# Kernel tuning notes

Hardware: AMD Instinct MI355X
Metric: run time of the kernel (lower is better)

The kernel has to match this reference:

```python
import jax, jax.numpy as jnp
import numpy as np

H, N, S, CH, LEN = 512, 64, 512, 1, 4096  # d_model, state size, n_ssm, channels, kernel length


def setup_inputs() -> dict:
    key = jax.random.key(0)
    k1, k2 = jax.random.split(key, 2)
    # dt ~ logUniform(1e-3, 1e-1), standard S4 init
    log_dt = jax.random.uniform(k1, (H,), minval=float(np.log(1e-3)),
                                maxval=float(np.log(1e-1))).astype(jnp.float32)
    # A = -0.5 + i*pi*n (S4D-Lin); stored as inv_A_real = log(-A.real) for real_type='exp'
    inv_A_real = jnp.full((S, N), float(np.log(0.5)), dtype=jnp.float32)
    A_imag = jnp.tile((np.pi * jnp.arange(N, dtype=jnp.float32))[None, :], (S, 1))
    # B = 1 + 0j, stored as real view (..., 2)
    B = jnp.stack([jnp.ones((S, N), jnp.float32), jnp.zeros((S, N), jnp.float32)], axis=-1)
    # C ~ complex normal with std 1/sqrt(2) per component, real view (CH, H, N, 2)
    C = (jax.random.normal(k2, (CH, H, N, 2)) * (0.5 ** 0.5)).astype(jnp.float32)
    return {"log_dt": log_dt, "C": C, "B": B, "inv_A_real": inv_A_real,
            "A_imag": A_imag, "L": LEN}


def _s4d_kernel(log_dt, C, B, inv_A_real, A_imag, L):
    """SSKernelDiag.forward with disc='zoh', real_type='exp', state=None, rate=1.0."""
    dt = jnp.exp(log_dt)                                   # (H,)
    Cc = C[..., 0] + 1j * C[..., 1]                        # (CH, H, N) complex
    Bc = B[..., 0] + 1j * B[..., 1]                        # (S, N) complex
    A = -jnp.exp(inv_A_real) + 1j * A_imag                 # (S, N) complex, Re(A)<0
    rep = H // A.shape[0]
    A = jnp.tile(A, (rep, 1))                              # (H, N)
    Bc = jnp.tile(Bc, (rep, 1))                            # (H, N)
    dtA = A * dt[:, None]                                  # (H, N)
    Cc = Bc[None, :, :] * Cc                               # (CH, H, N)
    Cc = Cc * (jnp.exp(dtA) - 1.0) / A                     # ZOH input discretization
    # log-Vandermonde: K[c,h,l] = 2*Re( sum_n C[c,h,n] * exp(dtA[h,n]*l) )
    ell = jnp.arange(L, dtype=jnp.float32)                 # (L,)
    V = jnp.exp(dtA[:, :, None] * ell)                     # (H, N, L) complex -- the big intermediate
    K = 2.0 * jnp.einsum('chn,hnl->chl', Cc, V).real       # (CH, H, L)
    return K.astype(jnp.float32)


def reference(log_dt, C, B, inv_A_real, A_imag, L):
    # Returns the convolution kernel K of shape (channels, H, L); K_state is None.
    return _s4d_kernel(log_dt, C, B, inv_A_real, A_imag, L)
```

## Files before the change

kernel.cpp:

```cpp
#include <hip/hip_runtime.h>
#include <math.h>

#define H_DIM  512
#define N_DIM  64
#define S_DIM  512
#define L_DIM  4096
#define BLOCK  256
#define KCH    16

__device__ __forceinline__ void cis_big(float th, float l, float& c, float& s) {
    double rev = (double)th * (double)l * 0.15915494309189535;
    rev -= floor(rev);
    float ang = (float)rev * 6.283185307179586f;
    __sincosf(ang, &s, &c);
}

__global__ __launch_bounds__(BLOCK) void s4d_kernel(
    const float* __restrict__ log_dt,
    const float* __restrict__ C,
    const float* __restrict__ B,
    const float* __restrict__ invA,
    const float* __restrict__ Aim,
    float* __restrict__ out)
{
    __shared__ float hdr[N_DIM][8];

    const int h   = blockIdx.x;
    const int tid = threadIdx.x;

    if (tid < N_DIM) {
        const int n  = tid;
        const int sn = (h % S_DIM) * N_DIM + n;
        const float dt  = __expf(log_dt[h]);
        const float Ar  = -__expf(invA[sn]);
        const float Ai  = Aim[sn];
        const float are = Ar * dt;
        const float aim = Ai * dt;

        const float e1 = __expf(are);
        const float s1 = sinf(aim);
        const float c1 = cosf(aim);
        const float Er = e1 * c1 - 1.0f;
        const float Ei = e1 * s1;

        const float inv = 1.0f / (Ar * Ar + Ai * Ai);
        const float Fr  = (Er * Ar + Ei * Ai) * inv;
        const float Fi  = (Ei * Ar - Er * Ai) * inv;

        const float Br = B[2 * sn], Bi = B[2 * sn + 1];
        const int  chn = h * N_DIM + n;
        const float Cr = C[2 * chn], Ci = C[2 * chn + 1];
        const float BCr = Br * Cr - Bi * Ci;
        const float BCi = Br * Ci + Bi * Cr;
        const float Gr = 2.0f * (BCr * Fr - BCi * Fi);
        const float Gi = 2.0f * (BCr * Fi + BCi * Fr);

        float cS, sS, c8, s8;
        cis_big(aim, (float)BLOCK, cS, sS);
        cis_big(aim, (float)(8 * BLOCK), c8, s8);
        const float eS = __expf(are * (float)BLOCK);
        const float e8 = __expf(are * (float)(8 * BLOCK));

        hdr[n][0] = eS * cS;
        hdr[n][1] = eS * sS;
        hdr[n][2] = e8 * c8;
        hdr[n][3] = e8 * s8;
        hdr[n][4] = Gr;
        hdr[n][5] = Gi;
        hdr[n][6] = are * 1.44269504088896f;
        hdr[n][7] = aim * 0.15915494309189535f;
    }
    __syncthreads();

    const float l0f = (float)tid;

    float acc[KCH];
#pragma unroll
    for (int k = 0; k < KCH; ++k) acc[k] = 0.0f;

    for (int n = 0; n < N_DIM; ++n) {
        const float4 h0 = *(const float4*)&hdr[n][0];
        const float4 h1 = *(const float4*)&hdr[n][4];

        float rev = h1.w * l0f;
        rev -= floorf(rev);
        float s, c;
        __sincosf(rev * 6.2831853071795864f, &s, &c);
        const float e0 = exp2f(h1.z * l0f);
        const float t0 = e0 * c, t1 = e0 * s;

        float ar = fmaf(h1.x, t0, -h1.y * t1);
        float ai = fmaf(h1.x, t1,  h1.y * t0);
        float br = fmaf(ar, h0.z, -ai * h0.w);
        float bi = fmaf(ar, h0.w,  ai * h0.z);

#pragma unroll
        for (int k = 0; k < 8; ++k) {
            acc[k]     += ar;
            acc[k + 8] += br;
            const float tA = fmaf(ar, h0.x, -ai * h0.y);
            ai             = fmaf(ar, h0.y,  ai * h0.x);
            ar             = tA;
            const float tB = fmaf(br, h0.x, -bi * h0.y);
            bi             = fmaf(br, h0.y,  bi * h0.x);
            br             = tB;
        }
    }

    float* o = out + h * L_DIM + tid;
#pragma unroll
    for (int k = 0; k < KCH; ++k) o[k * BLOCK] = acc[k];
}

extern "C" void kernel_launch(void* const* d_in, const int* in_sizes, int n_in,
                              void* d_out, int out_size, void* d_ws, size_t ws_size,
                              hipStream_t stream) {
    const float* log_dt = (const float*)d_in[0];
    const float* C      = (const float*)d_in[1];
    const float* B      = (const float*)d_in[2];
    const float* invA   = (const float*)d_in[3];
    const float* Aim    = (const float*)d_in[4];
    float* out = (float*)d_out;

    s4d_kernel<<<dim3(H_DIM), BLOCK, 0, stream>>>(log_dt, C, B, invA, Aim, out);
}
```

Baseline: 88.21 us.

## Split L across two blocks and use real-only second-order recurrence

Doubles the grid by giving each block half of the sequence length, with 8 outputs per thread instead of 16. The complex power recurrence becomes a real second-order linear recurrence y_{k+1} = 2Re(W) y_k - |W|^2 y_{k-1}, so only the real part is tracked. Per element this needs about one FMA plus one multiply instead of four complex-multiply ops. The aim is more parallelism (1024 blocks) and fewer ALU ops. In exchange the per-block header setup is duplicated, and the three-term recurrence may drift numerically differently.

```diff
diff --git a/kernel.cpp b/kernel.cpp
--- a/kernel.cpp
+++ b/kernel.cpp
@@ -6,7 +6,8 @@
 #define S_DIM  512
 #define L_DIM  4096
 #define BLOCK  256
-#define KCH    16
+#define KCH    8
+#define LSPLIT (L_DIM / (BLOCK * KCH))
 
 __device__ __forceinline__ void cis_big(float th, float l, float& c, float& s) {
     double rev = (double)th * (double)l * 0.15915494309189535;
@@ -26,6 +27,7 @@
     __shared__ float hdr[N_DIM][8];
 
     const int h   = blockIdx.x;
+    const int half = blockIdx.y;
     const int tid = threadIdx.x;
 
     if (tid < N_DIM) {
@@ -55,24 +57,24 @@
         const float Gr = 2.0f * (BCr * Fr - BCi * Fi);
         const float Gi = 2.0f * (BCr * Fi + BCi * Fr);
 
-        float cS, sS, c8, s8;
+        float cS, sS;
         cis_big(aim, (float)BLOCK, cS, sS);
-        cis_big(aim, (float)(8 * BLOCK), c8, s8);
         const float eS = __expf(are * (float)BLOCK);
-        const float e8 = __expf(are * (float)(8 * BLOCK));
+        const float Wr = eS * cS;
+        const float Wi = eS * sS;
 
-        hdr[n][0] = eS * cS;
-        hdr[n][1] = eS * sS;
-        hdr[n][2] = e8 * c8;
-        hdr[n][3] = e8 * s8;
-        hdr[n][4] = Gr;
-        hdr[n][5] = Gi;
-        hdr[n][6] = are * 1.44269504088896f;
-        hdr[n][7] = aim * 0.15915494309189535f;
+        hdr[n][0] = Wr;
+        hdr[n][1] = Wi;
+        hdr[n][2] = Wr + Wr;
+        hdr[n][3] = __expf(are * (float)(2 * BLOCK));
+        hdr[n][4] = are * 1.44269504088896f;
+        hdr[n][5] = aim * 0.15915494309189535f;
+        hdr[n][6] = Gr;
+        hdr[n][7] = Gi;
     }
     __syncthreads();
 
-    const float l0f = (float)tid;
+    const float l0f = (float)(half * (BLOCK * KCH) + tid);
 
     float acc[KCH];
 #pragma unroll
@@ -82,32 +84,29 @@
         const float4 h0 = *(const float4*)&hdr[n][0];
         const float4 h1 = *(const float4*)&hdr[n][4];
 
-        float rev = h1.w * l0f;
+        float rev = h1.y * l0f;
         rev -= floorf(rev);
         float s, c;
         __sincosf(rev * 6.2831853071795864f, &s, &c);
-        const float e0 = exp2f(h1.z * l0f);
+        const float e0 = exp2f(h1.x * l0f);
         const float t0 = e0 * c, t1 = e0 * s;
+        const float qr = fmaf(h1.z, t0, -h1.w * t1);
+        const float qi = fmaf(h1.z, t1,  h1.w * t0);
 
-        float ar = fmaf(h1.x, t0, -h1.y * t1);
-        float ai = fmaf(h1.x, t1,  h1.y * t0);
-        float br = fmaf(ar, h0.z, -ai * h0.w);
-        float bi = fmaf(ar, h0.w,  ai * h0.z);
-
+        float yp = qr;
+        float yc = fmaf(qr, h0.x, -qi * h0.y);
+        acc[0] += yp;
+        acc[1] += yc;
 #pragma unroll
-        for (int k = 0; k < 8; ++k) {
-            acc[k]     += ar;
-            acc[k + 8] += br;
-            const float tA = fmaf(ar, h0.x, -ai * h0.y);
-            ai             = fmaf(ar, h0.y,  ai * h0.x);
-            ar             = tA;
-            const float tB = fmaf(br, h0.x, -bi * h0.y);
-            bi             = fmaf(br, h0.y,  bi * h0.x);
-            br             = tB;
+        for (int k = 2; k < KCH; ++k) {
+            const float yn = fmaf(h0.z, yc, -h0.w * yp);
+            yp = yc;
+            yc = yn;
+            acc[k] += yn;
         }
     }
 
-    float* o = out + h * L_DIM + tid;
+    float* o = out + h * L_DIM + half * (BLOCK * KCH) + tid;
 #pragma unroll
     for (int k = 0; k < KCH; ++k) o[k * BLOCK] = acc[k];
 }
@@ -122,5 +121,5 @@
     const float* Aim    = (const float*)d_in[4];
     float* out = (float*)d_out;
 
-    s4d_kernel<<<dim3(H_DIM), BLOCK, 0, stream>>>(log_dt, C, B, invA, Aim, out);
+    s4d_kernel<<<dim3(H_DIM, LSPLIT), BLOCK, 0, stream>>>(log_dt, C, B, invA, Aim, out);
 }
```

After: 83.18 us. -5.7%, faster.
